# Kernel optimization log

Measured on AMD Instinct MI355X. Metric: run time of the kernel, lower is better.

Reference implementation:

```python
import jax, jax.numpy as jnp
import numpy as np

B, L, H = 64, 512, 1024


def _gen_masks():
    rng = np.random.default_rng(0)

    def gen_cat(items_lo, items_hi, w_lo, w_hi, s_lo, s_hi):
        items_per_ex = rng.integers(items_lo, items_hi + 1, size=B)
        word_counts, sub_counts = [], []
        ex_sub = np.zeros(B, np.int64)
        ex_word = np.zeros(B, np.int64)
        for i in range(B):
            for _ in range(int(items_per_ex[i])):
                nw = int(rng.integers(w_lo, w_hi + 1))
                word_counts.append(nw)
                ex_word[i] += nw
                for _ in range(nw):
                    ns = int(rng.integers(s_lo, s_hi + 1))
                    sub_counts.append(ns)
                    ex_sub[i] += ns
        return items_per_ex, np.array(word_counts), np.array(sub_counts), ex_sub, ex_word

    q = gen_cat(1, 1, 8, 15, 1, 3)     # one question per example
    t = gen_cat(3, 6, 1, 3, 1, 3)      # tables per example
    c = gen_cat(12, 25, 1, 4, 1, 3)    # columns per example

    def plm_mask(starts, lens):
        m = np.zeros((B, L), bool)
        for i in range(B):
            m[i, starts[i]:starts[i] + lens[i]] = True
        return m

    qs = np.ones(B, np.int64)
    ts = qs + q[3]
    cs = ts + t[3]
    assert int((cs + c[3]).max()) <= L

    def sub_mask(sc):
        return np.arange(sc.max())[None, :] < sc[:, None]

    masks = dict(
        question_mask_plm=plm_mask(qs, q[3]),
        table_mask_plm=plm_mask(ts, t[3]),
        column_mask_plm=plm_mask(cs, c[3]),
        question_subword_mask=sub_mask(q[2]),
        table_subword_mask=sub_mask(t[2]),
        column_subword_mask=sub_mask(c[2]),
        question_mask=np.arange(q[4].max())[None, :] < q[4][:, None],
        table_word_mask=np.arange(t[1].max())[None, :] < t[1][:, None],
        column_word_mask=np.arange(c[1].max())[None, :] < c[1][:, None],
    )
    return {k: jnp.asarray(v) for k, v in masks.items()}


def setup_inputs() -> dict:
    key = jax.random.key(0)
    k1, k2 = jax.random.split(key)
    inp = _gen_masks()
    inp["inputs"] = jax.random.normal(k1, (B, L, H), jnp.float32)
    inp["W"] = jax.random.normal(k2, (H, H), jnp.float32) * 0.02
    inp["b"] = jnp.zeros((H,), jnp.float32)
    return inp


def _move(values, src_mask, dst_mask):
    """masked_select(src_mask) followed by masked_scatter_(dst_mask):
    the k-th True of src_mask feeds the k-th True of dst_mask (row-major)."""
    Hd = values.shape[-1]
    v = values.reshape(-1, Hd)
    sm = src_mask.reshape(-1)
    n = v.shape[0]
    rank = jnp.cumsum(sm) - 1                       # rank among True positions
    buf = jnp.zeros((n, Hd), v.dtype).at[jnp.where(sm, rank, n)].set(v, mode="drop")
    dm = dst_mask.reshape(-1)
    drank = jnp.clip(jnp.cumsum(dm) - 1, 0, n - 1)
    out = jnp.where(dm[:, None], buf[drank], 0.0)
    return out.reshape(dst_mask.shape + (Hd,))


def _scatter_rows(rows, dst_mask):
    """masked_scatter_ of consecutive row vectors into True slots of dst_mask."""
    dm = dst_mask.reshape(-1)
    rank = jnp.clip(jnp.cumsum(dm) - 1, 0, rows.shape[0] - 1)
    out = jnp.where(dm[:, None], rows[rank], 0.0)
    return out.reshape(dst_mask.shape + (rows.shape[-1],))


def _pool(x, mask, W, b):
    # PoolingFunction(method='mean-pooling'): masked mean over subwords, then Linear+Tanh
    mf = mask.astype(x.dtype)[..., None]
    mean = (x * mf).sum(1) / mf.sum(1)
    return jnp.tanh(mean @ W.T + b)


def _forward(inputs, W, b, m):
    q = _pool(_move(inputs, m["question_mask_plm"], m["question_subword_mask"]),
              m["question_subword_mask"], W, b)
    t = _pool(_move(inputs, m["table_mask_plm"], m["table_subword_mask"]),
              m["table_subword_mask"], W, b)
    c = _pool(_move(inputs, m["column_mask_plm"], m["column_subword_mask"]),
              m["column_subword_mask"], W, b)
    return (_scatter_rows(q, m["question_mask"]),
            _scatter_rows(t, m["table_word_mask"]),
            _scatter_rows(c, m["column_word_mask"]))


def reference(inputs, W, b, question_mask_plm, table_mask_plm, column_mask_plm,
              question_subword_mask, table_subword_mask, column_subword_mask,
              question_mask, table_word_mask, column_word_mask):
    m = dict(question_mask_plm=question_mask_plm, table_mask_plm=table_mask_plm,
             column_mask_plm=column_mask_plm, question_subword_mask=question_subword_mask,
             table_subword_mask=table_subword_mask, column_subword_mask=column_subword_mask,
             question_mask=question_mask, table_word_mask=table_word_mask,
             column_word_mask=column_word_mask)
    return _forward(inputs, W, b, m)
```

## Files before the change

### kernel.cpp

```cpp
#include <hip/hip_runtime.h>
#include <hip/hip_bf16.h>
#include <stdint.h>

#define BB 64
#define LL 512
#define HH 1024

using short8 = __attribute__((ext_vector_type(8))) short;
using f32x4  = __attribute__((ext_vector_type(4))) float;

static __device__ __forceinline__ unsigned short f2b(float x) {
    union { float f; uint32_t u; } t; t.f = x;
    uint32_t u = t.u;
    u += 0x7fffu + ((u >> 16) & 1u);
    return (unsigned short)(u >> 16);
}

__global__ __launch_bounds__(256)
void meta_kernel(const int* __restrict__ plm0, const int* __restrict__ plm1,
                 const int* __restrict__ plm2,
                 const int* __restrict__ sub0, const int* __restrict__ sub1,
                 const int* __restrict__ sub2,
                 const int* __restrict__ wm0, const int* __restrict__ wm1,
                 const int* __restrict__ wm2,
                 int ssub0, int ssub1, int ssub2,
                 int wmsz0, int wmsz1, int wmsz2,
                 int cap0, int cap1, int cap2,
                 int* __restrict__ g_src, int* __restrict__ g_ns,
                 int* __restrict__ g_orow)
{
    const int cat = blockIdx.x;
    const int* P    = (cat == 0) ? plm0 : (cat == 1) ? plm1 : plm2;
    const int* D    = (cat == 0) ? sub0 : (cat == 1) ? sub1 : sub2;
    const int* WM   = (cat == 0) ? wm0  : (cat == 1) ? wm1  : wm2;
    const int ssub  = (cat == 0) ? ssub0 : (cat == 1) ? ssub1 : ssub2;
    const int wmsz  = (cat == 0) ? wmsz0 : (cat == 1) ? wmsz1 : wmsz2;
    const int cap   = (cat == 0) ? cap0  : (cat == 1) ? cap1  : cap2;
    int wb = 0, rbase = 0;
    if (cat >= 1) { wb += cap0; rbase += wmsz0; }
    if (cat >= 2) { wb += cap1; rbase += wmsz1; }

    __shared__ int ex_f[BB], ex_cnt[BB];
    __shared__ int ex_sub_off[BB + 1];
    __shared__ int scanbuf[256];
    __shared__ int carry_sh;
    __shared__ int NW_sh;

    const int tid = threadIdx.x;

    if (tid < BB) {
        const int* row = P + tid * LL;
        int f = -1, c = 0;
        for (int k = 0; k < LL; ++k) {
            int v = row[k];
            if (v) { ++c; if (f < 0) f = k; }
        }
        ex_f[tid] = (f < 0) ? 0 : f;
        ex_cnt[tid] = c;
    }
    __syncthreads();
    if (tid == 0) {
        int s = 0;
        for (int i = 0; i < BB; ++i) { ex_sub_off[i] = s; s += ex_cnt[i]; }
        ex_sub_off[BB] = s;
        carry_sh = 0;
    }
    __syncthreads();

    for (int base = 0; base < wmsz; base += 256) {
        const int p = base + tid;
        const int v = (p < wmsz) ? (WM[p] != 0) : 0;
        scanbuf[tid] = v;
        __syncthreads();
        for (int off = 1; off < 256; off <<= 1) {
            int x = (tid >= off) ? scanbuf[tid - off] : 0;
            __syncthreads();
            scanbuf[tid] += x;
            __syncthreads();
        }
        const int k = carry_sh + scanbuf[tid] - v;
        if (v) g_orow[wb + k] = rbase + p;
        __syncthreads();
        if (tid == 255) carry_sh += scanbuf[255];
        __syncthreads();
    }
    if (tid == 0) { NW_sh = carry_sh; carry_sh = 0; }
    __syncthreads();
    const int NW = NW_sh;
    const int Smax = (NW > 0) ? (ssub / NW) : 1;

    for (int k = NW + tid; k < cap; k += 256) {
        g_orow[wb + k] = -1;
        g_ns[wb + k] = 0;
        g_src[wb + k] = 0;
    }

    for (int base = 0; base < NW; base += 256) {
        const int w = base + tid;
        int ns = 0;
        if (w < NW) {
            const int* dr = D + (size_t)w * Smax;
            for (int j = 0; j < Smax; ++j) ns += (dr[j] != 0);
        }
        scanbuf[tid] = ns;
        __syncthreads();
        for (int off = 1; off < 256; off <<= 1) {
            int x = (tid >= off) ? scanbuf[tid - off] : 0;
            __syncthreads();
            scanbuf[tid] += x;
            __syncthreads();
        }
        const int subrank = carry_sh + scanbuf[tid] - ns;
        if (w < NW) {
            int lo = 0, hi = BB;
            while (hi - lo > 1) {
                int mid = (lo + hi) >> 1;
                if (ex_sub_off[mid] <= subrank) lo = mid; else hi = mid;
            }
            const int i = lo;
            const int gw = wb + w;
            g_src[gw] = i * LL + ex_f[i] + (subrank - ex_sub_off[i]);
            g_ns[gw]  = ns;
        }
        __syncthreads();
        if (tid == 255) carry_sh += scanbuf[255];
        __syncthreads();
    }
}

__global__ __launch_bounds__(256)
void means_kernel(const float* __restrict__ X, const int* __restrict__ g_src,
                  const int* __restrict__ g_ns, const int* __restrict__ g_orow,
                  unsigned short* __restrict__ meansB)
{
    const int w = blockIdx.x;
    if (g_orow[w] < 0) return;
    const int ns = g_ns[w];
    const int base = g_src[w];
    const int c0 = threadIdx.x * 4;
    float ax = 0.f, ay = 0.f, az = 0.f, aw = 0.f;
    for (int j = 0; j < ns; ++j) {
        const float4 v = *reinterpret_cast<const float4*>(
            X + (size_t)(base + j) * HH + c0);
        ax += v.x; ay += v.y; az += v.z; aw += v.w;
    }
    const float s = 1.0f / (float)ns;
    ushort4 o;
    o.x = f2b(ax * s); o.y = f2b(ay * s); o.z = f2b(az * s); o.w = f2b(aw * s);
    *reinterpret_cast<ushort4*>(meansB + (size_t)w * HH + c0) = o;
}

__global__ __launch_bounds__(256)
void wconv_kernel(const float* __restrict__ Wf, unsigned short* __restrict__ Wb)
{
    const int idx = (blockIdx.x * 256 + threadIdx.x) * 4;
    const float4 v = *reinterpret_cast<const float4*>(Wf + idx);
    ushort4 o;
    o.x = f2b(v.x); o.y = f2b(v.y); o.z = f2b(v.z); o.w = f2b(v.w);
    *reinterpret_cast<ushort4*>(Wb + idx) = o;
}

__global__ __launch_bounds__(256)
void gemm_kernel(const unsigned short* __restrict__ A,
                 const unsigned short* __restrict__ Wb,
                 const float* __restrict__ bias,
                 const int* __restrict__ g_orow,
                 float* __restrict__ out, int M_total)
{
    __shared__ unsigned short lb[64 * 40];

    const int m_base = blockIdx.x * 64;
    const int n_base = blockIdx.y * 64;
    const int tid = threadIdx.x;
    const int wv = tid >> 6;
    const int lane = tid & 63;
    const int q = lane >> 4;
    const int ml = lane & 15;

    const int row16 = m_base + wv * 16 + ml;
    const int orow_ml = (row16 < M_total) ? g_orow[row16] : -1;
    if (!__syncthreads_or(orow_ml >= 0)) return;

    f32x4 acc[4];
    #pragma unroll
    for (int t = 0; t < 4; ++t) acc[t] = (f32x4){0.f, 0.f, 0.f, 0.f};

    const int lrow = tid >> 2;
    const int lq = tid & 3;
    const unsigned short* Bsrc = Wb + (size_t)(n_base + lrow) * HH + lq * 8;
    unsigned short* Bdst = lb + lrow * 40 + lq * 8;

    const unsigned short* Ap = A + (size_t)row16 * HH + q * 8;
    const unsigned short* l0 = lb + ml * 40 + q * 8;

    for (int k0 = 0; k0 < HH; k0 += 32) {
        __syncthreads();
        *reinterpret_cast<short8*>(Bdst) =
            *reinterpret_cast<const short8*>(Bsrc + k0);
        __syncthreads();
        const short8 a  = *reinterpret_cast<const short8*>(Ap + k0);
        const short8 b0 = *reinterpret_cast<const short8*>(l0);
        const short8 b1 = *reinterpret_cast<const short8*>(l0 + 16 * 40);
        const short8 b2 = *reinterpret_cast<const short8*>(l0 + 32 * 40);
        const short8 b3 = *reinterpret_cast<const short8*>(l0 + 48 * 40);
        acc[0] = __builtin_amdgcn_mfma_f32_16x16x32_bf16(a, b0, acc[0], 0, 0, 0);
        acc[1] = __builtin_amdgcn_mfma_f32_16x16x32_bf16(a, b1, acc[1], 0, 0, 0);
        acc[2] = __builtin_amdgcn_mfma_f32_16x16x32_bf16(a, b2, acc[2], 0, 0, 0);
        acc[3] = __builtin_amdgcn_mfma_f32_16x16x32_bf16(a, b3, acc[3], 0, 0, 0);
    }

    #pragma unroll
    for (int t = 0; t < 4; ++t) {
        const int col = n_base + t * 16 + ml;
        const float bv = bias[col];
        #pragma unroll
        for (int r = 0; r < 4; ++r) {
            const int row = m_base + wv * 16 + q * 4 + r;
            if (row < M_total) {
                const int orow = g_orow[row];
                if (orow >= 0) {
                    out[(size_t)orow * HH + col] = tanhf(acc[t][r] + bv);
                }
            }
        }
    }
}

extern "C" void kernel_launch(void* const* d_in, const int* in_sizes, int n_in,
                              void* d_out, int out_size, void* d_ws, size_t ws_size,
                              hipStream_t stream)
{
    const int* plm0 = (const int*)d_in[0];
    const int* plm1 = (const int*)d_in[1];
    const int* plm2 = (const int*)d_in[2];
    const int* sub0 = (const int*)d_in[3];
    const int* sub1 = (const int*)d_in[4];
    const int* sub2 = (const int*)d_in[5];
    const int* wm0  = (const int*)d_in[6];
    const int* wm1  = (const int*)d_in[7];
    const int* wm2  = (const int*)d_in[8];
    const float* X    = (const float*)d_in[9];
    const float* Wf   = (const float*)d_in[10];
    const float* bias = (const float*)d_in[11];

    const int wmsz0 = in_sizes[6], wmsz1 = in_sizes[7], wmsz2 = in_sizes[8];
    const int cap0 = (wmsz0 + 63) & ~63;
    const int cap1 = (wmsz1 + 63) & ~63;
    const int cap2 = (wmsz2 + 63) & ~63;
    const int Mslots = cap0 + cap1 + cap2;
    const int gx = Mslots / 64;

    char* ws = (char*)d_ws;
    unsigned short* Wb = (unsigned short*)ws;
    unsigned short* meansB = (unsigned short*)(ws + (size_t)HH * HH * 2);
    char* p = ws + (size_t)HH * HH * 2 + (size_t)Mslots * HH * 2;
    int* g_src  = (int*)p; p += (size_t)Mslots * 4;
    int* g_ns   = (int*)p; p += (size_t)Mslots * 4;
    int* g_orow = (int*)p;

    hipMemsetAsync(d_out, 0, (size_t)out_size * sizeof(float), stream);

    wconv_kernel<<<(HH * HH / 4) / 256, 256, 0, stream>>>(Wf, Wb);

    meta_kernel<<<3, 256, 0, stream>>>(plm0, plm1, plm2, sub0, sub1, sub2,
                                       wm0, wm1, wm2,
                                       in_sizes[3], in_sizes[4], in_sizes[5],
                                       wmsz0, wmsz1, wmsz2,
                                       cap0, cap1, cap2,
                                       g_src, g_ns, g_orow);

    means_kernel<<<Mslots, 256, 0, stream>>>(X, g_src, g_ns, g_orow, meansB);

    gemm_kernel<<<dim3(gx, 16), 256, 0, stream>>>(meansB, Wb, bias, g_orow,
                                                  (float*)d_out, Mslots);
}
```

Baseline: 320.2 us.

## Parallelize metadata scans with wave shuffles and double GEMM K-step

The metadata kernel now splits the per-example PLM row scan across all 256 threads using int4 loads. Its block-wide scans, which used repeated __syncthreads, become per-thread serial segments combined with wavefront shuffle scans. The GEMM kernel stages 64 K elements of W per iteration instead of 32, with wider LDS rows, so it runs half as many barrier pairs and issues eight MFMAs between syncs. The cost is more LDS per block and serial per-thread segment loops, which may load-balance unevenly.

```diff
diff --git a/kernel.cpp b/kernel.cpp
--- a/kernel.cpp
+++ b/kernel.cpp
@@ -40,91 +40,107 @@
     if (cat >= 1) { wb += cap0; rbase += wmsz0; }
     if (cat >= 2) { wb += cap1; rbase += wmsz1; }
 
-    __shared__ int ex_f[BB], ex_cnt[BB];
+    __shared__ int ex_f[BB];
     __shared__ int ex_sub_off[BB + 1];
-    __shared__ int scanbuf[256];
-    __shared__ int carry_sh;
-    __shared__ int NW_sh;
+    __shared__ int qf[256], qc[256];
+    __shared__ int wsum[4];
 
     const int tid = threadIdx.x;
-
-    if (tid < BB) {
-        const int* row = P + tid * LL;
-        int f = -1, c = 0;
-        for (int k = 0; k < LL; ++k) {
-            int v = row[k];
-            if (v) { ++c; if (f < 0) f = k; }
-        }
-        ex_f[tid] = (f < 0) ? 0 : f;
-        ex_cnt[tid] = c;
-    }
-    __syncthreads();
-    if (tid == 0) {
-        int s = 0;
-        for (int i = 0; i < BB; ++i) { ex_sub_off[i] = s; s += ex_cnt[i]; }
-        ex_sub_off[BB] = s;
-        carry_sh = 0;
-    }
-    __syncthreads();
-
-    for (int base = 0; base < wmsz; base += 256) {
-        const int p = base + tid;
-        const int v = (p < wmsz) ? (WM[p] != 0) : 0;
-        scanbuf[tid] = v;
-        __syncthreads();
-        for (int off = 1; off < 256; off <<= 1) {
-            int x = (tid >= off) ? scanbuf[tid - off] : 0;
-            __syncthreads();
-            scanbuf[tid] += x;
-            __syncthreads();
-        }
-        const int k = carry_sh + scanbuf[tid] - v;
-        if (v) g_orow[wb + k] = rbase + p;
-        __syncthreads();
-        if (tid == 255) carry_sh += scanbuf[255];
-        __syncthreads();
-    }
-    if (tid == 0) { NW_sh = carry_sh; carry_sh = 0; }
-    __syncthreads();
-    const int NW = NW_sh;
+    const int lane = tid & 63;
+    const int wv = tid >> 6;
+
+    {
+        const int row = tid & 63;
+        const int quarter = tid >> 6;
+        const int4* rp = reinterpret_cast<const int4*>(P + row * LL + quarter * 128);
+        int c = 0, f = 0x7fffffff;
+        #pragma unroll 8
+        for (int i = 0; i < 32; ++i) {
+            int4 v = rp[i];
+            if (v.x) { ++c; if (f == 0x7fffffff) f = quarter * 128 + i * 4 + 0; }
+            if (v.y) { ++c; if (f == 0x7fffffff) f = quarter * 128 + i * 4 + 1; }
+            if (v.z) { ++c; if (f == 0x7fffffff) f = quarter * 128 + i * 4 + 2; }
+            if (v.w) { ++c; if (f == 0x7fffffff) f = quarter * 128 + i * 4 + 3; }
+        }
+        qc[tid] = c;
+        qf[tid] = f;
+    }
+    __syncthreads();
+    if (tid < 64) {
+        int c = qc[tid] + qc[tid + 64] + qc[tid + 128] + qc[tid + 192];
+        int f = min(min(qf[tid], qf[tid + 64]), min(qf[tid + 128], qf[tid + 192]));
+        ex_f[tid] = (f == 0x7fffffff) ? 0 : f;
+        int v = c;
+        #pragma unroll
+        for (int off = 1; off < 64; off <<= 1) {
+            int u = __shfl_up(v, off, 64);
+            if (tid >= off) v += u;
+        }
+        ex_sub_off[tid + 1] = v;
+        if (tid == 0) ex_sub_off[0] = 0;
+    }
+    __syncthreads();
+
+    const int seg = (wmsz + 255) >> 8;
+    const int p0 = tid * seg;
+    const int p1 = min(p0 + seg, wmsz);
+    int c = 0;
+    for (int p = p0; p < p1; ++p) c += (WM[p] != 0);
+    int incl = c;
+    #pragma unroll
+    for (int off = 1; off < 64; off <<= 1) {
+        int u = __shfl_up(incl, off, 64);
+        if (lane >= off) incl += u;
+    }
+    if (lane == 63) wsum[wv] = incl;
+    __syncthreads();
+    int woff = 0;
+    for (int i = 0; i < wv; ++i) woff += wsum[i];
+    const int NW = wsum[0] + wsum[1] + wsum[2] + wsum[3];
+    int k = woff + incl - c;
+    for (int p = p0; p < p1; ++p)
+        if (WM[p]) g_orow[wb + (k++)] = rbase + p;
+
+    for (int w = NW + tid; w < cap; w += 256) {
+        g_orow[wb + w] = -1;
+        g_ns[wb + w] = 0;
+        g_src[wb + w] = 0;
+    }
+
     const int Smax = (NW > 0) ? (ssub / NW) : 1;
 
-    for (int k = NW + tid; k < cap; k += 256) {
-        g_orow[wb + k] = -1;
-        g_ns[wb + k] = 0;
-        g_src[wb + k] = 0;
-    }
-
-    for (int base = 0; base < NW; base += 256) {
-        const int w = base + tid;
+    const int seg2 = (NW + 255) >> 8;
+    const int w0 = tid * seg2;
+    const int w1 = min(w0 + seg2, NW);
+    int cs = 0;
+    for (int w = w0; w < w1; ++w) {
+        const int* dr = D + (size_t)w * Smax;
+        for (int j = 0; j < Smax; ++j) cs += (dr[j] != 0);
+    }
+    __syncthreads();
+    int incl2 = cs;
+    #pragma unroll
+    for (int off = 1; off < 64; off <<= 1) {
+        int u = __shfl_up(incl2, off, 64);
+        if (lane >= off) incl2 += u;
+    }
+    if (lane == 63) wsum[wv] = incl2;
+    __syncthreads();
+    int soff = 0;
+    for (int i = 0; i < wv; ++i) soff += wsum[i];
+    int subrank = soff + incl2 - cs;
+    for (int w = w0; w < w1; ++w) {
         int ns = 0;
-        if (w < NW) {
-            const int* dr = D + (size_t)w * Smax;
-            for (int j = 0; j < Smax; ++j) ns += (dr[j] != 0);
-        }
-        scanbuf[tid] = ns;
-        __syncthreads();
-        for (int off = 1; off < 256; off <<= 1) {
-            int x = (tid >= off) ? scanbuf[tid - off] : 0;
-            __syncthreads();
-            scanbuf[tid] += x;
-            __syncthreads();
-        }
-        const int subrank = carry_sh + scanbuf[tid] - ns;
-        if (w < NW) {
-            int lo = 0, hi = BB;
-            while (hi - lo > 1) {
-                int mid = (lo + hi) >> 1;
-                if (ex_sub_off[mid] <= subrank) lo = mid; else hi = mid;
-            }
-            const int i = lo;
-            const int gw = wb + w;
-            g_src[gw] = i * LL + ex_f[i] + (subrank - ex_sub_off[i]);
-            g_ns[gw]  = ns;
-        }
-        __syncthreads();
-        if (tid == 255) carry_sh += scanbuf[255];
-        __syncthreads();
+        const int* dr = D + (size_t)w * Smax;
+        for (int j = 0; j < Smax; ++j) ns += (dr[j] != 0);
+        int lo = 0, hi = BB;
+        while (hi - lo > 1) {
+            int mid = (lo + hi) >> 1;
+            if (ex_sub_off[mid] <= subrank) lo = mid; else hi = mid;
+        }
+        g_src[wb + w] = lo * LL + ex_f[lo] + (subrank - ex_sub_off[lo]);
+        g_ns[wb + w] = ns;
+        subrank += ns;
     }
 }
 
@@ -167,7 +183,7 @@
                  const int* __restrict__ g_orow,
                  float* __restrict__ out, int M_total)
 {
-    __shared__ unsigned short lb[64 * 40];
+    __shared__ unsigned short lb[64 * 72];
 
     const int m_base = blockIdx.x * 64;
     const int n_base = blockIdx.y * 64;
@@ -185,28 +201,33 @@
     #pragma unroll
     for (int t = 0; t < 4; ++t) acc[t] = (f32x4){0.f, 0.f, 0.f, 0.f};
 
-    const int lrow = tid >> 2;
-    const int lq = tid & 3;
-    const unsigned short* Bsrc = Wb + (size_t)(n_base + lrow) * HH + lq * 8;
-    unsigned short* Bdst = lb + lrow * 40 + lq * 8;
+    const int srow = tid >> 2;
+    const int schunk = tid & 3;
+    const unsigned short* Bsrc = Wb + (size_t)(n_base + srow) * HH + schunk * 16;
+    unsigned short* Bdst = lb + srow * 72 + schunk * 16;
 
     const unsigned short* Ap = A + (size_t)row16 * HH + q * 8;
-    const unsigned short* l0 = lb + ml * 40 + q * 8;
-
-    for (int k0 = 0; k0 < HH; k0 += 32) {
+    const unsigned short* l0 = lb + ml * 72 + q * 8;
+
+    for (int k0 = 0; k0 < HH; k0 += 64) {
         __syncthreads();
         *reinterpret_cast<short8*>(Bdst) =
             *reinterpret_cast<const short8*>(Bsrc + k0);
+        *reinterpret_cast<short8*>(Bdst + 8) =
+            *reinterpret_cast<const short8*>(Bsrc + k0 + 8);
         __syncthreads();
-        const short8 a  = *reinterpret_cast<const short8*>(Ap + k0);
-        const short8 b0 = *reinterpret_cast<const short8*>(l0);
-        const short8 b1 = *reinterpret_cast<const short8*>(l0 + 16 * 40);
-        const short8 b2 = *reinterpret_cast<const short8*>(l0 + 32 * 40);
-        const short8 b3 = *reinterpret_cast<const short8*>(l0 + 48 * 40);
-        acc[0] = __builtin_amdgcn_mfma_f32_16x16x32_bf16(a, b0, acc[0], 0, 0, 0);
-        acc[1] = __builtin_amdgcn_mfma_f32_16x16x32_bf16(a, b1, acc[1], 0, 0, 0);
-        acc[2] = __builtin_amdgcn_mfma_f32_16x16x32_bf16(a, b2, acc[2], 0, 0, 0);
-        acc[3] = __builtin_amdgcn_mfma_f32_16x16x32_bf16(a, b3, acc[3], 0, 0, 0);
+        const short8 a0 = *reinterpret_cast<const short8*>(Ap + k0);
+        const short8 a1 = *reinterpret_cast<const short8*>(Ap + k0 + 32);
+        #pragma unroll
+        for (int nq = 0; nq < 4; ++nq) {
+            const short8 b0 = *reinterpret_cast<const short8*>(l0 + nq * 16 * 72);
+            acc[nq] = __builtin_amdgcn_mfma_f32_16x16x32_bf16(a0, b0, acc[nq], 0, 0, 0);
+        }
+        #pragma unroll
+        for (int nq = 0; nq < 4; ++nq) {
+            const short8 b1 = *reinterpret_cast<const short8*>(l0 + nq * 16 * 72 + 32);
+            acc[nq] = __builtin_amdgcn_mfma_f32_16x16x32_bf16(a1, b1, acc[nq], 0, 0, 0);
+        }
     }
 
     #pragma unroll
```

Measured after the change: 281.2 us. 1.14x faster.
